# Optimization experiments

Measured on AMD Instinct MI355X. Metric: run time of the kernel, lower is better.

## Reference

```python
import jax, jax.numpy as jnp
import numpy as np


def _gat_layer(h, mask, w, a_src, a_dst):
    # h: [B,C,N,Fin], w: [C,H,Fin,Fout], a_*: [C,H,Fout,1], mask: [B,N,N] (True where no edge)
    h_prime = jnp.einsum('bcni,chio->bchno', h, w)          # [B,C,H,N,Fout]
    t = jnp.tanh(h_prime)
    s = jnp.einsum('bchno,cho->bchn', t, a_src[..., 0])      # src scores
    d = jnp.einsum('bchno,cho->bchn', t, a_dst[..., 0])      # dst scores
    attn = s[..., :, None] + d[..., None, :]                 # [B,C,H,N,N]
    attn = jnp.where(attn >= 0, attn, 0.2 * attn)            # leaky_relu(0.2)
    attn = jnp.where(mask[:, None, None, :, :], jnp.float32(-1e12), attn)
    attn = jax.nn.softmax(attn, axis=-1)
    return jnp.einsum('bchnm,bchmo->bchno', attn, h_prime)   # [B,C,H,N,Fout]


def setup_inputs() -> dict:
    key = jax.random.key(0)
    ks = jax.random.split(key, 8)
    B, C, N, F0, H, F = 2, 2, 1024, 64, 8, 64

    def xavier(k, shape):
        fan_in, fan_out = shape[-2], shape[-1]
        lim = (6.0 / (fan_in + fan_out)) ** 0.5
        return jax.random.uniform(k, shape, jnp.float32, -lim, lim)

    x = jax.random.normal(ks[0], (B, C, N, F0), dtype=jnp.float32)
    adj = jax.random.randint(ks[1], (B, N, N), 0, 2, dtype=jnp.int32)
    w1 = xavier(ks[2], (C, H, F0, F))
    a_src1 = xavier(ks[3], (C, H, F, 1))
    a_dst1 = xavier(ks[4], (C, H, F, 1))
    w2 = xavier(ks[5], (C, H, H * F, F))
    a_src2 = xavier(ks[6], (C, H, F, 1))
    a_dst2 = xavier(ks[7], (C, H, F, 1))
    return {"x": x, "adj": adj, "w1": w1, "a_src1": a_src1, "a_dst1": a_dst1,
            "w2": w2, "a_src2": a_src2, "a_dst2": a_dst2}


def reference(x, adj, w1, a_src1, a_dst1, w2, a_src2, a_dst2):
    B, C, N, _ = x.shape
    adj_f = adj.astype(jnp.float32) + jnp.eye(N, dtype=jnp.float32)[None]  # add self-loops
    mask = adj_f == 0                                        # [B,N,N]
    out1 = _gat_layer(x, mask, w1, a_src1, a_dst1)           # [B,C,H,N,F]
    # permute heads next to features, flatten, elu (dropout is identity in eval)
    x1 = jax.nn.elu(jnp.transpose(out1, (0, 1, 3, 2, 4)).reshape(B, C, N, -1))
    out2 = _gat_layer(x1, mask, w2, a_src2, a_dst2)          # [B,C,H,N,F]
    return out2.mean(axis=2)                                 # mean over heads -> [B,C,N,F]
```

## Files before the change

### kernel.cpp

```cpp
#include <hip/hip_runtime.h>

#define BB 2
#define CC 2
#define NN 1024
#define HH 8
#define BCHN 32
#define SVN  (BCHN*NN)
#define LOG2E 1.44269504f

typedef _Float16 f16x8 __attribute__((ext_vector_type(8)));
typedef _Float16 f16x4 __attribute__((ext_vector_type(4)));
typedef __fp16 h16x2 __attribute__((ext_vector_type(2)));
typedef float f32x4 __attribute__((ext_vector_type(4)));

__device__ __forceinline__ float fexp2(float x) {
  float r; asm("v_exp_f32 %0, %1" : "=v"(r) : "v"(x)); return r;
}

__device__ __forceinline__ void gl_lds16(const _Float16* g, _Float16* l) {
  __builtin_amdgcn_global_load_lds(
      (const __attribute__((address_space(1))) void*)g,
      (__attribute__((address_space(3))) void*)l, 16, 0, 0);
}


__global__ __launch_bounds__(256) void proj1_fused(
    const float* __restrict__ x, const int* __restrict__ adj,
    const float* __restrict__ w1, const float* __restrict__ w2,
    const float* __restrict__ asrc, const float* __restrict__ adst,
    _Float16* __restrict__ w2T, unsigned long long* __restrict__ bmg,
    _Float16* __restrict__ HpT, float* __restrict__ s_out, float* __restrict__ d_out)
{
  __shared__ union {
    __align__(16) _Float16 tile[64*72];
    struct { float sp[4][32]; float sd[4][32]; } pr;
  } sm;
  const int bx = blockIdx.x;
  const int t = threadIdx.x;
  const int w = t >> 6, lane = t & 63;
  const int colr = lane & 15, quad = lane >> 4;

  if (bx < 1024) {
    const int bch = bx & 31;
    const int row0 = (bx >> 5) * 32;
    const int h = bch & 7; const int bc = bch >> 3; const int c = bc & 1;

    const float* Ar0 = x + ((size_t)bc*NN + row0 + colr)*64;
    const float* Ar1 = Ar0 + (size_t)16*64;
    const float* Bw  = w1 + ((size_t)(c*HH + h))*64*64 + w*16 + colr;

    f32x4 acc0 = {0.f,0.f,0.f,0.f}, acc1 = {0.f,0.f,0.f,0.f};
    #pragma unroll
    for (int kb = 0; kb < 64; kb += 32) {
      const float4 pa0 = *(const float4*)(Ar0 + kb + quad*8);
      const float4 pa1 = *(const float4*)(Ar0 + kb + quad*8 + 4);
      const float4 pb0 = *(const float4*)(Ar1 + kb + quad*8);
      const float4 pb1 = *(const float4*)(Ar1 + kb + quad*8 + 4);
      float bv[8];
      #pragma unroll
      for (int j = 0; j < 8; ++j) bv[j] = Bw[(size_t)(kb + quad*8 + j)*64];
      f16x8 a0, a1, bf;
      a0[0]=(_Float16)pa0.x; a0[1]=(_Float16)pa0.y; a0[2]=(_Float16)pa0.z; a0[3]=(_Float16)pa0.w;
      a0[4]=(_Float16)pa1.x; a0[5]=(_Float16)pa1.y; a0[6]=(_Float16)pa1.z; a0[7]=(_Float16)pa1.w;
      a1[0]=(_Float16)pb0.x; a1[1]=(_Float16)pb0.y; a1[2]=(_Float16)pb0.z; a1[3]=(_Float16)pb0.w;
      a1[4]=(_Float16)pb1.x; a1[5]=(_Float16)pb1.y; a1[6]=(_Float16)pb1.z; a1[7]=(_Float16)pb1.w;
      #pragma unroll
      for (int j = 0; j < 8; ++j) bf[j] = (_Float16)bv[j];
      acc0 = __builtin_amdgcn_mfma_f32_16x16x32_f16(a0, bf, acc0, 0, 0, 0);
      acc1 = __builtin_amdgcn_mfma_f32_16x16x32_f16(a1, bf, acc1, 0, 0, 0);
    }

    const float af  = asrc[(c*HH + h)*64 + w*16 + colr];
    const float bf_ = adst[(c*HH + h)*64 + w*16 + colr];
    _Float16* HT = HpT + (size_t)bch*65536 + (size_t)(row0 >> 5)*2048;

    #pragma unroll
    for (int mt = 0; mt < 2; ++mt) {
      const f32x4 a = mt ? acc1 : acc0;
      f16x4 hv;
      #pragma unroll
      for (int i = 0; i < 4; ++i) {
        const float v = a[i];
        hv[i] = (_Float16)v;
        const float ex = __expf(2.f*v);
        const float th = 1.f - 2.f/(ex + 1.f);
        float ps = th * af, pd = th * bf_;
        #pragma unroll
        for (int off = 1; off < 16; off <<= 1) {
          ps += __shfl_xor(ps, off);
          pd += __shfl_xor(pd, off);
        }
        if (colr == 0) {
          sm.pr.sp[w][mt*16 + quad*4 + i] = ps;
          sm.pr.sd[w][mt*16 + quad*4 + i] = pd;
        }
      }
      const int chunk = w*64 + (mt*2 + (quad >> 1))*16 + colr;
      *(f16x4*)(HT + chunk*8 + (quad & 1)*4) = hv;
    }
    __syncthreads();
    if (t < 32) {
      const float sv = sm.pr.sp[0][t] + sm.pr.sp[1][t] + sm.pr.sp[2][t] + sm.pr.sp[3][t];
      const float dv = sm.pr.sd[0][t] + sm.pr.sd[1][t] + sm.pr.sd[2][t] + sm.pr.sd[3][t];
      s_out[bch*NN + row0 + t] = sv * LOG2E;
      d_out[bch*NN + row0 + t] = dv * LOG2E;
    }
  } else if (bx < 1152) {
    const int u = bx - 1024;
    const int ch = u >> 3, k0 = (u & 7)*64;
    const float* src = w2 + ((size_t)ch*512 + k0)*64;
    #pragma unroll
    for (int j = 0; j < 4; ++j) {
      const int uu = t + j*256;
      const int k = uu >> 4, seg = uu & 15;
      const float4 v = ((const float4*)src)[(size_t)k*16 + seg];
      sm.tile[(seg*4+0)*72 + k] = (_Float16)v.x;
      sm.tile[(seg*4+1)*72 + k] = (_Float16)v.y;
      sm.tile[(seg*4+2)*72 + k] = (_Float16)v.z;
      sm.tile[(seg*4+3)*72 + k] = (_Float16)v.w;
    }
    __syncthreads();
    _Float16* dst = w2T + (size_t)ch*32768;
    #pragma unroll
    for (int j = 0; j < 2; ++j) {
      const int uu = t + j*256;
      const int f = uu >> 3, seg = uu & 7;
      const f16x8 o = *(const f16x8*)&sm.tile[f*72 + seg*8];
      const int kk = k0 + seg*8;
      const int chunk = (f >> 4)*64 + ((seg & 3))*16 + (f & 15);
      *(f16x8*)(dst + (size_t)(kk >> 5)*2048 + chunk*8) = o;
    }
  } else {
    const int g = (bx - 1152)*4 + w;
    const int base = g*32;
    #pragma unroll
    for (int jb = 0; jb < 4; ++jb) {
      int vals[8];
      #pragma unroll
      for (int i = 0; i < 8; ++i) {
        const int idx = base + jb*8 + i;
        const int b = idx >> 14;
        const int n = (idx >> 4) & (NN - 1);
        const int wd = idx & 15;
        vals[i] = adj[((size_t)b*NN + n)*NN + wd*64 + lane];
      }
      #pragma unroll
      for (int i = 0; i < 8; ++i) {
        const int idx = base + jb*8 + i;
        const int n = (idx >> 4) & (NN - 1);
        const int m = (idx & 15)*64 + lane;
        const unsigned long long bits = __ballot((vals[i] != 0) || (m == n));
        if (lane == 0) bmg[idx] = bits;
      }
    }
  }
}

template<int LAYER>
__global__ __launch_bounds__(1024, 4) void attn_monster(
    const _Float16* __restrict__ HpTin, const float* __restrict__ s_arr,
    const float* __restrict__ d_arr, const unsigned long long* __restrict__ bmg,
    const _Float16* __restrict__ w2T, const float* __restrict__ asrc2,
    const float* __restrict__ adst2,
    _Float16* __restrict__ HpT2, float* __restrict__ s2, float* __restrict__ d2,
    float* __restrict__ out)
{
  __shared__ union {
    struct {
      __align__(16) _Float16 stg[2][16][2048];
      __align__(16) float dstg[16][512];
    } kl;
    struct {
      float obuf[2][8][16][68];
      float dsb[2][8][16];
      float spb[8][16], sdb[8][16];
      __align__(16) _Float16 x1[8192];
      __align__(16) _Float16 wstg[2][16][1024];
    } l1;
    struct { float mbuf[16][64]; float dsb[2][8][16]; } l2;
  } sm;

  const int bc = blockIdx.x;
  const int r0 = blockIdx.y * 16;
  const int t = threadIdx.x;
  const int wv = t >> 6;
  const int h  = wv >> 1, kh = wv & 1;
  const int lane = t & 63;
  const int colr = lane & 15, quad = lane >> 4;
  const int bch = bc*HH + h;
  const int b = bc >> 1, c = bc & 1;

  const float* dg = d_arr + (size_t)bch*NN;
  const float4* dg4 = (const float4*)dg;
  float mxl = -1e30f;
  #pragma unroll
  for (int j = 0; j < 4; ++j) {
    const float4 v = dg4[lane + 64*j];
    mxl = fmaxf(fmaxf(v.x, v.y), fmaxf(fmaxf(v.z, v.w), mxl));
  }
  #pragma unroll
  for (int off = 1; off < 64; off <<= 1) mxl = fmaxf(mxl, __shfl_xor(mxl, off));
  const float maxd = mxl;

  const int r = r0 + colr;
  const float s = s_arr[(size_t)bch*NN + r];
  const float so = s + maxd;
  const float offs = fmaxf(so, 0.2f*so);
  const float sA = s - offs, sB = 0.2f*s - offs;

  unsigned long long m[8];
  {
    const unsigned long long* bm = bmg + ((size_t)b*NN + r)*16 + kh*8;
    #pragma unroll
    for (int j = 0; j < 8; ++j) m[j] = bm[j];
  }

  {
    const float4* s4 = (const float4*)(dg + kh*512);
    const float4 v0 = s4[lane*2];
    const float4 v1 = s4[lane*2 + 1];
    *(float4*)&sm.kl.dstg[wv][lane*8]     = v0;
    *(float4*)&sm.kl.dstg[wv][lane*8 + 4] = v1;
  }

  const _Float16* strip = HpTin + (size_t)bch*65536 + (size_t)kh*32768;

  f32x4 acc[4];
  f32x4 accs = {0.f,0.f,0.f,0.f};
  #pragma unroll
  for (int ft = 0; ft < 4; ++ft) acc[ft] = (f32x4){0.f,0.f,0.f,0.f};
  f16x8 ones;
  #pragma unroll
  for (int i = 0; i < 8; ++i) ones[i] = (_Float16)1.f;

#define STAGE_B(tt) { \
    const _Float16* gs_ = strip + (tt)*2048 + lane*8; \
    _Float16* ls_ = &sm.kl.stg[(tt) & 1][wv][0]; \
    gl_lds16(gs_,        ls_); \
    gl_lds16(gs_ + 512,  ls_ + 512); \
    gl_lds16(gs_ + 1024, ls_ + 1024); \
    gl_lds16(gs_ + 1536, ls_ + 1536); }

  STAGE_B(0);

  #pragma unroll
  for (int ks = 0; ks < 16; ++ks) {
    if (ks < 15) {
      asm volatile("s_waitcnt lgkmcnt(0)" ::: "memory");
      STAGE_B(ks + 1);
      asm volatile("s_waitcnt vmcnt(4)" ::: "memory");
    } else {
      asm volatile("s_waitcnt vmcnt(0)" ::: "memory");
    }

    f16x8 Bc[4];
    #pragma unroll
    for (int ft = 0; ft < 4; ++ft)
      Bc[ft] = *(const f16x8*)&sm.kl.stg[ks & 1][wv][ft*512 + lane*8];

    const float* dls = &sm.kl.dstg[wv][ks*32 + quad*8];
    const float4 da0 = *(const float4*)dls;
    const float4 da1 = *(const float4*)(dls + 4);

    __builtin_amdgcn_s_setprio(1);
    const unsigned mb = (unsigned)((m[ks >> 1] >> ((ks & 1)*32 + quad*8)) & 0xFFull);
    const float dd[8] = {da0.x, da0.y, da0.z, da0.w, da1.x, da1.y, da1.z, da1.w};
    union { f16x8 v; h16x2 hh[4]; } A;
    #pragma unroll
    for (int jp = 0; jp < 4; ++jp) {
      float p[2];
      #pragma unroll
      for (int jj = 0; jj < 2; ++jj) {
        const int j = jp*2 + jj;
        const float dj = dd[j];
        const float l = fmaxf(sA + dj, fmaf(0.2f, dj, sB));
        p[jj] = ((mb >> j) & 1u) ? fexp2(l) : 0.f;
      }
      A.hh[jp] = __builtin_amdgcn_cvt_pkrtz(p[0], p[1]);
    }
    #pragma unroll
    for (int ft = 0; ft < 4; ++ft)
      acc[ft] = __builtin_amdgcn_mfma_f32_16x16x32_f16(A.v, Bc[ft], acc[ft], 0, 0, 0);
    accs = __builtin_amdgcn_mfma_f32_16x16x32_f16(A.v, ones, accs, 0, 0, 0);
    __builtin_amdgcn_s_setprio(0);
  }
#undef STAGE_B

  __syncthreads();

  if (LAYER == 1) {
    if (t < 256) (&sm.l1.spb[0][0])[t] = 0.f;
    #pragma unroll
    for (int ft = 0; ft < 4; ++ft)
      #pragma unroll
      for (int i = 0; i < 4; ++i)
        sm.l1.obuf[kh][h][quad*4 + i][ft*16 + colr] = acc[ft][i];
    if (colr == 0) {
      #pragma unroll
      for (int i = 0; i < 4; ++i) sm.l1.dsb[kh][h][quad*4 + i] = accs[i];
    }
    __syncthreads();

    {
      const int row = t >> 6;
      const int hp  = (t >> 3) & 7;
      const int f0  = (t & 7)*8;
      const float invd = 1.f / (sm.l1.dsb[0][hp][row] + sm.l1.dsb[1][hp][row]);
      const float* ob0 = &sm.l1.obuf[0][hp][row][f0];
      const float* ob1 = &sm.l1.obuf[1][hp][row][f0];
      f16x8 xo;
      #pragma unroll
      for (int j = 0; j < 8; ++j) {
        float v = (ob0[j] + ob1[j]) * invd;
        v = v > 0.f ? v : expm1f(v);
        xo[j] = (_Float16)v;
      }
      const int chunk = (hp*2 + (f0 >> 5))*64 + ((f0 >> 3) & 3)*16 + row;
      *(f16x8*)&sm.l1.x1[chunk*8] = xo;
    }
    __syncthreads();

    const int fb = kh*2;
    const _Float16* wstrip = w2T + (size_t)(c*HH + h)*32768 + fb*512;
    f32x4 acc2[2];
    acc2[0] = (f32x4){0.f,0.f,0.f,0.f}; acc2[1] = (f32x4){0.f,0.f,0.f,0.f};

#define STAGE_W(tt) { \
    const _Float16* gs_ = wstrip + (tt)*2048 + lane*8; \
    _Float16* ls_ = &sm.l1.wstg[(tt) & 1][wv][0]; \
    gl_lds16(gs_,       ls_); \
    gl_lds16(gs_ + 512, ls_ + 512); }

    STAGE_W(0);
    #pragma unroll
    for (int k2 = 0; k2 < 16; ++k2) {
      if (k2 < 15) {
        asm volatile("s_waitcnt lgkmcnt(0)" ::: "memory");
        STAGE_W(k2 + 1);
        asm volatile("s_waitcnt vmcnt(2)" ::: "memory");
      } else {
        asm volatile("s_waitcnt vmcnt(0)" ::: "memory");
      }
      f16x8 Wc[2];
      #pragma unroll
      for (int u = 0; u < 2; ++u)
        Wc[u] = *(const f16x8*)&sm.l1.wstg[k2 & 1][wv][u*512 + lane*8];
      const f16x8 Af = *(const f16x8*)&sm.l1.x1[(k2*64 + lane)*8];
      #pragma unroll
      for (int u = 0; u < 2; ++u)
        acc2[u] = __builtin_amdgcn_mfma_f32_16x16x32_f16(Af, Wc[u], acc2[u], 0, 0, 0);
    }
#undef STAGE_W

    float af[2], bfv[2];
    #pragma unroll
    for (int u = 0; u < 2; ++u) {
      af[u]  = asrc2[(c*HH + h)*64 + (fb+u)*16 + colr];
      bfv[u] = adst2[(c*HH + h)*64 + (fb+u)*16 + colr];
    }
    #pragma unroll
    for (int i = 0; i < 4; ++i) {
      float ps = 0.f, pd = 0.f;
      #pragma unroll
      for (int u = 0; u < 2; ++u) {
        const float v = acc2[u][i];
        const float ex = __expf(2.f*v);
        const float th = 1.f - 2.f/(ex + 1.f);
        ps += th * af[u]; pd += th * bfv[u];
      }
      #pragma unroll
      for (int off = 1; off < 16; off <<= 1) {
        ps += __shfl_xor(ps, off);
        pd += __shfl_xor(pd, off);
      }
      if (colr == 0) {
        atomicAdd(&sm.l1.spb[h][quad*4 + i], ps);
        atomicAdd(&sm.l1.sdb[h][quad*4 + i], pd);
      }
    }
    _Float16* H2 = HpT2 + (size_t)bch*65536 + (size_t)(r0 >> 5)*2048;
    const int kgb = 2*((r0 >> 4) & 1) + (quad >> 1);
    #pragma unroll
    for (int u = 0; u < 2; ++u) {
      f16x4 hv;
      #pragma unroll
      for (int i = 0; i < 4; ++i) hv[i] = (_Float16)acc2[u][i];
      const int chunk = (fb+u)*64 + kgb*16 + colr;
      *(f16x4*)(H2 + chunk*8 + (quad & 1)*4) = hv;
    }
    __syncthreads();
    if (t < 128) {
      const int hp = t >> 4, rr = t & 15;
      s2[(size_t)(bc*HH + hp)*NN + r0 + rr] = sm.l1.spb[hp][rr] * LOG2E;
      d2[(size_t)(bc*HH + hp)*NN + r0 + rr] = sm.l1.sdb[hp][rr] * LOG2E;
    }
  } else {
    sm.l2.mbuf[t >> 6][t & 63] = 0.f;
    if (colr == 0) {
      #pragma unroll
      for (int i = 0; i < 4; ++i) sm.l2.dsb[kh][h][quad*4 + i] = accs[i];
    }
    __syncthreads();
    float inv[4];
    #pragma unroll
    for (int i = 0; i < 4; ++i)
      inv[i] = 0.125f / (sm.l2.dsb[0][h][quad*4 + i] + sm.l2.dsb[1][h][quad*4 + i]);
    #pragma unroll
    for (int ft = 0; ft < 4; ++ft)
      #pragma unroll
      for (int i = 0; i < 4; ++i)
        atomicAdd(&sm.l2.mbuf[quad*4 + i][ft*16 + colr], acc[ft][i] * inv[i]);
    __syncthreads();
    out[((size_t)bc*NN + r0 + wv)*64 + lane] = sm.l2.mbuf[wv][lane];
  }
}

extern "C" void kernel_launch(void* const* d_in, const int* in_sizes, int n_in,
                              void* d_out, int out_size, void* d_ws, size_t ws_size,
                              hipStream_t stream)
{
  const float* x   = (const float*)d_in[0];
  const int*   adj = (const int*)d_in[1];
  const float* w1  = (const float*)d_in[2];
  const float* as1 = (const float*)d_in[3];
  const float* ad1 = (const float*)d_in[4];
  const float* w2  = (const float*)d_in[5];
  const float* as2 = (const float*)d_in[6];
  const float* ad2 = (const float*)d_in[7];

  char* w8 = (char*)d_ws;
  _Float16* HpT  = (_Float16*)(w8);
  _Float16* HpT2 = (_Float16*)(w8 + (4u<<20));
  _Float16* w2T  = (_Float16*)(w8 + (8u<<20));
  float* s_v  = (float*)(w8 + (10u<<20));
  float* d_v  = (float*)(w8 + (10u<<20) + SVN*4);
  float* s2_v = (float*)(w8 + (10u<<20) + SVN*8);
  float* d2_v = (float*)(w8 + (10u<<20) + SVN*12);
  unsigned long long* bmg = (unsigned long long*)(w8 + (10u<<20) + SVN*16);

  proj1_fused<<<1408, 256, 0, stream>>>(x, adj, w1, w2, as1, ad1, w2T, bmg, HpT, s_v, d_v);
  attn_monster<1><<<dim3(4, 64), 1024, 0, stream>>>(HpT, s_v, d_v, bmg, w2T, as2, ad2,
                                                    HpT2, s2_v, d2_v, (float*)d_out);
  attn_monster<2><<<dim3(4, 64), 1024, 0, stream>>>(HpT2, s2_v, d2_v, bmg, w2T, as2, ad2,
                                                    HpT2, s2_v, d2_v, (float*)d_out);
}
```

Measured before the change: 151.1 us.

## Split layer-2 attention into per-head cooperative kernel plus head-reduction kernel

Replaces the layer-2 path of the monolithic attention kernel with a separate 256-thread kernel gridded over (batch·channel·head, 64-row tiles). Each block streams its head's projected features through double-buffered LDS via direct global-to-LDS loads and computes masked softmax-weighted MFMA products. It writes per-head fp16 results to a workspace, and a second small kernel sums the heads into the output. The goal is more parallelism and less LDS atomic contention than the 4x64-block monster launch. The cost is an extra launch, an fp16 intermediate round trip through global memory, and some lost precision in the head outputs.

```diff
diff --git a/kernel.cpp b/kernel.cpp
--- a/kernel.cpp
+++ b/kernel.cpp
@@ -394,25 +394,151 @@
       s2[(size_t)(bc*HH + hp)*NN + r0 + rr] = sm.l1.spb[hp][rr] * LOG2E;
       d2[(size_t)(bc*HH + hp)*NN + r0 + rr] = sm.l1.sdb[hp][rr] * LOG2E;
     }
-  } else {
-    sm.l2.mbuf[t >> 6][t & 63] = 0.f;
-    if (colr == 0) {
-      #pragma unroll
-      for (int i = 0; i < 4; ++i) sm.l2.dsb[kh][h][quad*4 + i] = accs[i];
-    }
-    __syncthreads();
-    float inv[4];
+  }
+}
+
+__global__ __launch_bounds__(256) void attn2_coop(
+    const _Float16* __restrict__ HpT2, const float* __restrict__ s_arr,
+    const float* __restrict__ d_arr, const unsigned long long* __restrict__ bmg,
+    _Float16* __restrict__ XB)
+{
+  __shared__ struct {
+    __align__(16) _Float16 stg[2][2048];
+    __align__(16) float dstg[1024];
+    float pw[4][16][68];
+  } sm;
+  const int bch = blockIdx.x;
+  const int r0 = blockIdx.y * 64;
+  const int t = threadIdx.x;
+  const int wv = t >> 6, lane = t & 63;
+  const int colr = lane & 15, quad = lane >> 4;
+  const int b = bch >> 4;
+
+  const float* dg = d_arr + (size_t)bch*NN;
+  const float4* dg4 = (const float4*)dg;
+  float mxl = -1e30f;
+  #pragma unroll
+  for (int j = 0; j < 4; ++j) {
+    const float4 v = dg4[lane + 64*j];
+    mxl = fmaxf(fmaxf(v.x, v.y), fmaxf(fmaxf(v.z, v.w), mxl));
+  }
+  #pragma unroll
+  for (int off = 1; off < 64; off <<= 1) mxl = fmaxf(mxl, __shfl_xor(mxl, off));
+  const float maxd = mxl;
+
+  *(float4*)&sm.dstg[t*4] = dg4[t];
+
+  const int r = r0 + wv*16 + colr;
+  const float s = s_arr[(size_t)bch*NN + r];
+  const float so = s + maxd;
+  const float offs = fmaxf(so, 0.2f*so);
+  const float sA = s - offs, sB = 0.2f*s - offs;
+
+  unsigned long long m[16];
+  {
+    const unsigned long long* bm = bmg + ((size_t)b*NN + r)*16;
+    #pragma unroll
+    for (int j = 0; j < 16; ++j) m[j] = bm[j];
+  }
+
+  const _Float16* strip = HpT2 + (size_t)bch*65536;
+
+  f32x4 acc[4];
+  f32x4 accs = {0.f,0.f,0.f,0.f};
+  #pragma unroll
+  for (int ft = 0; ft < 4; ++ft) acc[ft] = (f32x4){0.f,0.f,0.f,0.f};
+  f16x8 ones;
+  #pragma unroll
+  for (int i = 0; i < 8; ++i) ones[i] = (_Float16)1.f;
+
+  asm volatile("s_waitcnt vmcnt(0) lgkmcnt(0)" ::: "memory");
+  __builtin_amdgcn_s_barrier();
+
+#define STAGE_T(tt) \
+    gl_lds16(strip + (size_t)(tt)*2048 + wv*512 + lane*8, &sm.stg[(tt) & 1][wv*512]);
+
+  STAGE_T(0);
+  asm volatile("s_waitcnt vmcnt(0)" ::: "memory");
+  __builtin_amdgcn_s_barrier();
+
+  #pragma unroll 4
+  for (int ks = 0; ks < 32; ++ks) {
+    if (ks < 31) STAGE_T(ks + 1);
+
+    f16x8 Bc[4];
+    #pragma unroll
+    for (int ft = 0; ft < 4; ++ft)
+      Bc[ft] = *(const f16x8*)&sm.stg[ks & 1][ft*512 + lane*8];
+    const float* dls = &sm.dstg[ks*32 + quad*8];
+    const float4 da0 = *(const float4*)dls;
+    const float4 da1 = *(const float4*)(dls + 4);
+    asm volatile("s_waitcnt lgkmcnt(0)" ::: "memory");
+    __builtin_amdgcn_sched_barrier(0);
+
+    __builtin_amdgcn_s_setprio(1);
+    const unsigned mb = (unsigned)((m[ks >> 1] >> ((ks & 1)*32 + quad*8)) & 0xFFull);
+    const float dd[8] = {da0.x, da0.y, da0.z, da0.w, da1.x, da1.y, da1.z, da1.w};
+    union { f16x8 v; h16x2 hh[4]; } A;
+    #pragma unroll
+    for (int jp = 0; jp < 4; ++jp) {
+      float p[2];
+      #pragma unroll
+      for (int jj = 0; jj < 2; ++jj) {
+        const int j = jp*2 + jj;
+        const float dj = dd[j];
+        const float l = fmaxf(sA + dj, fmaf(0.2f, dj, sB));
+        p[jj] = ((mb >> j) & 1u) ? fexp2(l) : 0.f;
+      }
+      A.hh[jp] = __builtin_amdgcn_cvt_pkrtz(p[0], p[1]);
+    }
+    #pragma unroll
+    for (int ft = 0; ft < 4; ++ft)
+      acc[ft] = __builtin_amdgcn_mfma_f32_16x16x32_f16(A.v, Bc[ft], acc[ft], 0, 0, 0);
+    accs = __builtin_amdgcn_mfma_f32_16x16x32_f16(A.v, ones, accs, 0, 0, 0);
+    __builtin_amdgcn_s_setprio(0);
+
+    if (ks < 31) asm volatile("s_waitcnt vmcnt(0)" ::: "memory");
+    __builtin_amdgcn_s_barrier();
+  }
+#undef STAGE_T
+
+  float inv[4];
+  #pragma unroll
+  for (int i = 0; i < 4; ++i) inv[i] = 0.125f / accs[i];
+  float (*pw)[68] = sm.pw[wv];
+  #pragma unroll
+  for (int ft = 0; ft < 4; ++ft)
     #pragma unroll
     for (int i = 0; i < 4; ++i)
-      inv[i] = 0.125f / (sm.l2.dsb[0][h][quad*4 + i] + sm.l2.dsb[1][h][quad*4 + i]);
-    #pragma unroll
-    for (int ft = 0; ft < 4; ++ft)
-      #pragma unroll
-      for (int i = 0; i < 4; ++i)
-        atomicAdd(&sm.l2.mbuf[quad*4 + i][ft*16 + colr], acc[ft][i] * inv[i]);
-    __syncthreads();
-    out[((size_t)bc*NN + r0 + wv)*64 + lane] = sm.l2.mbuf[wv][lane];
-  }
+      pw[quad*4 + i][ft*16 + colr] = acc[ft][i] * inv[i];
+  const int row = lane >> 2, f0 = (lane & 3)*16;
+  f16x8 o0, o1;
+  #pragma unroll
+  for (int j = 0; j < 8; ++j) {
+    o0[j] = (_Float16)pw[row][f0 + j];
+    o1[j] = (_Float16)pw[row][f0 + 4 + ((j + 4) & 7)];
+  }
+  #pragma unroll
+  for (int j = 0; j < 8; ++j) o0[j] = (_Float16)pw[row][f0 + j];
+  #pragma unroll
+  for (int j = 0; j < 8; ++j) o1[j] = (_Float16)pw[row][f0 + 8 + j];
+  _Float16* dst = XB + ((size_t)bch*NN + r0 + wv*16 + row)*64 + f0;
+  *(f16x8*)dst = o0;
+  *(f16x8*)(dst + 8) = o1;
+}
+
+__global__ __launch_bounds__(256) void reduce_heads(
+    const _Float16* __restrict__ out2, float* __restrict__ out)
+{
+  const int o = blockIdx.x*256 + threadIdx.x;
+  const int f = o & 63;
+  const int n = (o >> 6) & (NN - 1);
+  const int bc = o >> 16;
+  float acc = 0.f;
+  #pragma unroll
+  for (int h = 0; h < HH; ++h)
+    acc += (float)out2[(((size_t)bc*HH + h)*NN + n)*64 + f];
+  out[o] = acc;
 }
 
 extern "C" void kernel_launch(void* const* d_in, const int* in_sizes, int n_in,
@@ -437,10 +563,11 @@
   float* s2_v = (float*)(w8 + (10u<<20) + SVN*8);
   float* d2_v = (float*)(w8 + (10u<<20) + SVN*12);
   unsigned long long* bmg = (unsigned long long*)(w8 + (10u<<20) + SVN*16);
+  _Float16* XB = (_Float16*)(w8 + (16u<<20));
 
   proj1_fused<<<1408, 256, 0, stream>>>(x, adj, w1, w2, as1, ad1, w2T, bmg, HpT, s_v, d_v);
   attn_monster<1><<<dim3(4, 64), 1024, 0, stream>>>(HpT, s_v, d_v, bmg, w2T, as2, ad2,
                                                     HpT2, s2_v, d2_v, (float*)d_out);
-  attn_monster<2><<<dim3(4, 64), 1024, 0, stream>>>(HpT2, s2_v, d2_v, bmg, w2T, as2, ad2,
-                                                    HpT2, s2_v, d2_v, (float*)d_out);
-}
+  attn2_coop<<<dim3(BCHN, NN/64), 256, 0, stream>>>(HpT2, s2_v, d2_v, bmg, XB);
+  reduce_heads<<<dim3((unsigned)(out_size/256)), 256, 0, stream>>>(XB, (float*)d_out);
+}
```

Result: faster. 138.0 us (-8.7%).
